# Performance work log

Hardware: AMD Instinct MI355X
Metric: run time of the kernel (lower is better)

## Reference

```python
import jax, jax.numpy as jnp
import numpy as np

BODY = 10      # inds_objs[0][0]
FEAT = 15      # len(inds_objs[0])
NOBJ = 8
HALF = 130     # dimo // 2
B = 65536


def _obj_idx():
    # column indices for each object's features: [NOBJ, 2*FEAT]
    base = BODY + FEAT * np.arange(NOBJ)[:, None] + np.arange(FEAT)[None, :]  # [NOBJ, FEAT]
    return jnp.asarray(np.concatenate([base, base + HALF], axis=1))           # [NOBJ, 30]


def setup_inputs() -> dict:
    key = jax.random.key(0)
    ks = jax.random.split(key, 9)
    def w(k, shape):
        fan_in = shape[0]
        return jax.random.normal(k, shape, jnp.float32) * (1.0 / np.sqrt(fan_in))
    return {
        "o": jax.random.normal(ks[0], (B, 260), jnp.float32),
        "g": jax.random.normal(ks[1], (B, 100), jnp.float32),
        "W_cast": w(ks[2], (100, 50)), "b_cast": jnp.zeros((50,), jnp.float32),
        "W_a0": w(ks[3], (50, 256)),   "b_a0": jnp.zeros((256,), jnp.float32),
        "W_a1": w(ks[4], (256, 400)),  "b_a1": jnp.zeros((400,), jnp.float32),
        "W_p0": w(ks[5], (400, 256)),  "b_p0": jnp.zeros((256,), jnp.float32),
        "W_p1": w(ks[6], (256, 256)),  "b_p1": jnp.zeros((256,), jnp.float32),
        "W_p2": w(ks[7], (256, 8)),    "b_p2": jnp.zeros((8,), jnp.float32),
    }


def reference(o, g, W_cast, b_cast, W_a0, b_a0, W_a1, b_a1,
              W_p0, b_p0, W_p1, b_p1, W_p2, b_p2):
    # attention gate from goal encoding: [B, 50]
    attention = jax.nn.sigmoid(g @ W_cast + b_cast)
    # body features (pos + vel halves): [B, 20]
    obs_body = jnp.concatenate([o[:, :BODY], o[:, HALF:HALF + BODY]], axis=1)
    # per-object features gathered in one shot: [B, NOBJ, 30]
    obs_obj = o[:, _obj_idx()]
    # concat body with each object: [B, NOBJ, 50]
    x = jnp.concatenate(
        [jnp.broadcast_to(obs_body[:, None, :], (o.shape[0], NOBJ, 2 * BODY)), obs_obj],
        axis=2)
    # elementwise attention gate (shared across objects)
    x = x * attention[:, None, :]
    # fc_actor: 50 -> 256 (relu) -> 400, then extra relu from forward()
    h = jax.nn.relu(jnp.einsum('bnd,dh->bnh', x, W_a0) + b_a0)
    y = jax.nn.relu(jnp.einsum('bnh,hk->bnk', h, W_a1) + b_a1)
    # deepset sum over objects: [B, 400]
    input_pi = y.sum(axis=1)
    # fc_pi: 400 -> 256 (relu) -> 256 (relu) -> 8, then tanh
    p = jax.nn.relu(input_pi @ W_p0 + b_p0)
    p = jax.nn.relu(p @ W_p1 + b_p1)
    return jnp.tanh(p @ W_p2 + b_p2)
```

## Files before the change

### kernel.cpp

```cpp
#include <hip/hip_runtime.h>
#include <hip/hip_bf16.h>

typedef _Float16 f16;
typedef f16 v8h __attribute__((ext_vector_type(8)));
typedef float v4f __attribute__((ext_vector_type(4)));
typedef unsigned short u16;

__device__ __forceinline__ u16 f2h(float f) {
  f16 h = (f16)f;
  return __builtin_bit_cast(unsigned short, h);
}
__device__ __forceinline__ float h2f(u16 u) {
  f16 h = __builtin_bit_cast(f16, u);
  return (float)h;
}
#define MFMA16(a, b, c) __builtin_amdgcn_mfma_f32_16x16x32_f16((a), (b), (c), 0, 0, 0)

__global__ void prep_weights(const float* __restrict__ Wc, const float* __restrict__ Wa0,
                             const float* __restrict__ Wa1, const float* __restrict__ Wp0,
                             const float* __restrict__ Wp1, const float* __restrict__ Wp2,
                             u16* __restrict__ ws) {
  int idx = blockIdx.x * 256 + threadIdx.x;
  float v;
  if (idx < 8192) {
    int n = idx >> 7, k = idx & 127;
    v = (n < 50 && k < 100) ? Wc[k * 50 + n] : 0.f;
  } else if (idx < 24576) {
    int i = idx - 8192; int n = i >> 6, k = i & 63;
    v = (k < 50) ? Wa0[k * 256 + n] : 0.f;
  } else if (idx < 126976) {
    int i = idx - 24576; int n = i >> 8, k = i & 255;
    v = Wa1[k * 400 + n];
  } else if (idx < 233472) {
    int i = idx - 126976; int n = i / 416, k = i - n * 416;
    v = (k < 400) ? Wp0[k * 256 + n] : 0.f;
  } else if (idx < 299008) {
    int i = idx - 233472; int n = i >> 8, k = i & 255;
    v = Wp1[k * 256 + n];
  } else if (idx < 303104) {
    int i = idx - 299008; int n = i >> 8, k = i & 255;
    v = (n < 8) ? Wp2[k * 8 + n] : 0.f;
  } else {
    return;
  }
  ws[idx] = f2h(v);
}

__global__ __launch_bounds__(1024) void actor_kernel(
    const float* __restrict__ o, const float* __restrict__ g,
    const float* __restrict__ b_cast, const float* __restrict__ b_a0,
    const float* __restrict__ b_a1, const float* __restrict__ b_p0,
    const float* __restrict__ b_p1, const float* __restrict__ b_p2,
    const u16* __restrict__ wsb, float* __restrict__ out) {
  __shared__ __align__(16) char smem[54272];
  u16* sAtt = (u16*)smem;
  u16* sG   = (u16*)(smem + 7168);
  u16* sX   = (u16*)(smem + 7168);
  u16* sH   = (u16*)(smem + 16384);
  u16* sY   = (u16*)smem;
  u16* sP   = (u16*)smem;

  const u16* WcT  = wsb;
  const u16* Wa0T = wsb + 8192;
  const u16* Wa1T = wsb + 24576;
  const u16* Wp0T = wsb + 126976;
  const u16* Wp1T = wsb + 233472;
  const u16* Wp2T = wsb + 299008;

  const int tid  = threadIdx.x;
  const int lane = tid & 63;
  const int w    = tid >> 6;
  const int nl   = lane & 15;
  const int q    = lane >> 4;
  const int row0 = blockIdx.x * 64;

  for (int idx = tid; idx < 64 * 128; idx += 1024) {
    int r = idx >> 7, c = idx & 127;
    float v = (c < 100) ? __builtin_nontemporal_load(&g[(row0 + r) * 100 + c]) : 0.f;
    sG[r * 136 + c] = f2h(v);
  }
  __syncthreads();

  {
    const int rb = w >> 2, nb = w & 3;
    const int col = nb * 16 + nl;
    v4f acc = {};
#pragma unroll
    for (int kb = 0; kb < 4; ++kb) {
      v8h bh = *(const v8h*)(WcT + col * 128 + kb * 32 + q * 8);
      v8h a  = *(const v8h*)&sG[(rb * 16 + nl) * 136 + kb * 32 + q * 8];
      acc = MFMA16(a, bh, acc);
    }
    if (col < 50) {
      float bias = b_cast[col];
#pragma unroll
      for (int rg = 0; rg < 4; ++rg) {
        float v = acc[rg] + bias;
        v = 1.f / (1.f + __expf(-v));
        sAtt[(rb * 16 + q * 4 + rg) * 56 + col] = f2h(v);
      }
    }
  }
  __syncthreads();

  for (int idx = tid; idx < 64 * 20; idx += 1024) {
    int r = idx / 20, c = idx - r * 20;
    int src = (c < 10) ? c : (c + 120);
    float v = __builtin_nontemporal_load(&o[(row0 + r) * 260 + src]) * h2f(sAtt[r * 56 + c]);
    sX[r * 72 + c] = f2h(v);
  }
  for (int idx = tid; idx < 64 * 14; idx += 1024) {
    int r = idx / 14, c = idx - r * 14;
    sX[r * 72 + 50 + c] = 0;
  }

  const int  nb0  = w;
  const int  nb1  = w + 16;
  const bool has1 = (nb1 < 25);
  const float biasA0  = b_a0[w * 16 + nl];
  const float biasA10 = b_a1[nb0 * 16 + nl];
  const float biasA11 = has1 ? b_a1[nb1 * 16 + nl] : 0.f;
  v4f y0[4] = {};
  v4f y1[4] = {};

  for (int obj = 0; obj < 8; ++obj) {
    for (int idx = tid; idx < 64 * 30; idx += 1024) {
      int r = idx / 30, j = idx - r * 30;
      int src = (j < 15) ? (10 + 15 * obj + j) : (125 + 15 * obj + j);
      float v = __builtin_nontemporal_load(&o[(row0 + r) * 260 + src]) * h2f(sAtt[r * 56 + 20 + j]);
      sX[r * 72 + 20 + j] = f2h(v);
    }
    __syncthreads();

    {
      v4f acc[4] = {};
#pragma unroll
      for (int kb = 0; kb < 2; ++kb) {
        v8h b0 = *(const v8h*)(Wa0T + (w * 16 + nl) * 64 + kb * 32 + q * 8);
#pragma unroll
        for (int rb = 0; rb < 4; ++rb) {
          v8h a = *(const v8h*)&sX[(rb * 16 + nl) * 72 + kb * 32 + q * 8];
          acc[rb] = MFMA16(a, b0, acc[rb]);
        }
      }
      const int col = w * 16 + nl;
#pragma unroll
      for (int rb = 0; rb < 4; ++rb)
#pragma unroll
        for (int rg = 0; rg < 4; ++rg) {
          float v = acc[rb][rg] + biasA0;
          v = v > 0.f ? v : 0.f;
          sH[(rb * 16 + q * 4 + rg) * 264 + col] = f2h(v);
        }
    }
    __syncthreads();

    {
      v4f t0[4] = {}, t1[4] = {};
#pragma unroll
      for (int kb = 0; kb < 8; ++kb) {
        v8h b0 = *(const v8h*)(Wa1T + (nb0 * 16 + nl) * 256 + kb * 32 + q * 8);
        v8h b1;
        if (has1) b1 = *(const v8h*)(Wa1T + (nb1 * 16 + nl) * 256 + kb * 32 + q * 8);
#pragma unroll
        for (int rb = 0; rb < 4; ++rb) {
          v8h a = *(const v8h*)&sH[(rb * 16 + nl) * 264 + kb * 32 + q * 8];
          t0[rb] = MFMA16(a, b0, t0[rb]);
          if (has1) t1[rb] = MFMA16(a, b1, t1[rb]);
        }
      }
#pragma unroll
      for (int rb = 0; rb < 4; ++rb)
#pragma unroll
        for (int rg = 0; rg < 4; ++rg) {
          float v = t0[rb][rg] + biasA10;
          y0[rb][rg] += (v > 0.f ? v : 0.f);
        }
      if (has1) {
#pragma unroll
        for (int rb = 0; rb < 4; ++rb)
#pragma unroll
          for (int rg = 0; rg < 4; ++rg) {
            float v = t1[rb][rg] + biasA11;
            y1[rb][rg] += (v > 0.f ? v : 0.f);
          }
      }
    }
  }
  __syncthreads();

  for (int idx = tid; idx < 64 * 16; idx += 1024) {
    int r = idx >> 4, c = idx & 15;
    sY[r * 424 + 400 + c] = 0;
  }
#pragma unroll
  for (int rb = 0; rb < 4; ++rb)
#pragma unroll
    for (int rg = 0; rg < 4; ++rg) {
      const int row = rb * 16 + q * 4 + rg;
      sY[row * 424 + nb0 * 16 + nl] = f2h(y0[rb][rg]);
      if (has1) sY[row * 424 + nb1 * 16 + nl] = f2h(y1[rb][rg]);
    }
  __syncthreads();

  v4f p0acc[4] = {};
#pragma unroll
  for (int kb = 0; kb < 13; ++kb) {
    v8h b0 = *(const v8h*)(Wp0T + (w * 16 + nl) * 416 + kb * 32 + q * 8);
#pragma unroll
    for (int rb = 0; rb < 4; ++rb) {
      v8h a = *(const v8h*)&sY[(rb * 16 + nl) * 424 + kb * 32 + q * 8];
      p0acc[rb] = MFMA16(a, b0, p0acc[rb]);
    }
  }
  __syncthreads();
  {
    const int col = w * 16 + nl;
    float bias = b_p0[col];
#pragma unroll
    for (int rb = 0; rb < 4; ++rb)
#pragma unroll
      for (int rg = 0; rg < 4; ++rg) {
        float v = p0acc[rb][rg] + bias;
        v = v > 0.f ? v : 0.f;
        sP[(rb * 16 + q * 4 + rg) * 264 + col] = f2h(v);
      }
  }
  __syncthreads();

  v4f p1acc[4] = {};
#pragma unroll
  for (int kb = 0; kb < 8; ++kb) {
    v8h b0 = *(const v8h*)(Wp1T + (w * 16 + nl) * 256 + kb * 32 + q * 8);
#pragma unroll
    for (int rb = 0; rb < 4; ++rb) {
      v8h a = *(const v8h*)&sP[(rb * 16 + nl) * 264 + kb * 32 + q * 8];
      p1acc[rb] = MFMA16(a, b0, p1acc[rb]);
    }
  }
  __syncthreads();
  {
    const int col = w * 16 + nl;
    float bias = b_p1[col];
#pragma unroll
    for (int rb = 0; rb < 4; ++rb)
#pragma unroll
      for (int rg = 0; rg < 4; ++rg) {
        float v = p1acc[rb][rg] + bias;
        v = v > 0.f ? v : 0.f;
        sP[(rb * 16 + q * 4 + rg) * 264 + col] = f2h(v);
      }
  }
  __syncthreads();

  if (w < 4) {
    v4f acc = {};
#pragma unroll
    for (int kb = 0; kb < 8; ++kb) {
      v8h a = *(const v8h*)&sP[(w * 16 + nl) * 264 + kb * 32 + q * 8];
      v8h b = *(const v8h*)(Wp2T + nl * 256 + kb * 32 + q * 8);
      acc = MFMA16(a, b, acc);
    }
    if (nl < 8) {
      float bias = b_p2[nl];
#pragma unroll
      for (int rg = 0; rg < 4; ++rg)
        __builtin_nontemporal_store(tanhf(acc[rg] + bias),
                                    &out[(row0 + w * 16 + q * 4 + rg) * 8 + nl]);
    }
  }
}

extern "C" void kernel_launch(void* const* d_in, const int* in_sizes, int n_in,
                              void* d_out, int out_size, void* d_ws, size_t ws_size,
                              hipStream_t stream) {
  const float* o   = (const float*)d_in[0];
  const float* g   = (const float*)d_in[1];
  const float* Wc  = (const float*)d_in[2];
  const float* bc  = (const float*)d_in[3];
  const float* Wa0 = (const float*)d_in[4];
  const float* ba0 = (const float*)d_in[5];
  const float* Wa1 = (const float*)d_in[6];
  const float* ba1 = (const float*)d_in[7];
  const float* Wp0 = (const float*)d_in[8];
  const float* bp0 = (const float*)d_in[9];
  const float* Wp1 = (const float*)d_in[10];
  const float* bp1 = (const float*)d_in[11];
  const float* Wp2 = (const float*)d_in[12];
  const float* bp2 = (const float*)d_in[13];
  u16* ws = (u16*)d_ws;
  float* out = (float*)d_out;

  int rows = in_sizes[0] / 260;

  prep_weights<<<1184, 256, 0, stream>>>(Wc, Wa0, Wa1, Wp0, Wp1, Wp2, ws);
  actor_kernel<<<rows / 64, 1024, 0, stream>>>(o, g, bc, ba0, ba1, bp0, bp1, bp2, ws, out);
}
```

Baseline: 379.3 us.

## Preload all object features into LDS, double-buffer hidden, transpose MFMA outputs for packed stores

```diff
diff --git a/kernel.cpp b/kernel.cpp
--- a/kernel.cpp
+++ b/kernel.cpp
@@ -4,7 +4,10 @@
 typedef _Float16 f16;
 typedef f16 v8h __attribute__((ext_vector_type(8)));
 typedef float v4f __attribute__((ext_vector_type(4)));
+typedef float v2f __attribute__((ext_vector_type(2)));
+typedef unsigned int v2u __attribute__((ext_vector_type(2)));
 typedef unsigned short u16;
+typedef unsigned int u32;
 
 __device__ __forceinline__ u16 f2h(float f) {
   f16 h = (f16)f;
@@ -13,6 +16,9 @@
 __device__ __forceinline__ float h2f(u16 u) {
   f16 h = __builtin_bit_cast(f16, u);
   return (float)h;
+}
+__device__ __forceinline__ u32 pk2(float a, float b) {
+  return (u32)f2h(a) | ((u32)f2h(b) << 16);
 }
 #define MFMA16(a, b, c) __builtin_amdgcn_mfma_f32_16x16x32_f16((a), (b), (c), 0, 0, 0)
 
@@ -52,13 +58,14 @@
     const float* __restrict__ b_a1, const float* __restrict__ b_p0,
     const float* __restrict__ b_p1, const float* __restrict__ b_p2,
     const u16* __restrict__ wsb, float* __restrict__ out) {
-  __shared__ __align__(16) char smem[54272];
+  __shared__ __align__(16) char smem[148480];
   u16* sAtt = (u16*)smem;
   u16* sG   = (u16*)(smem + 7168);
-  u16* sX   = (u16*)(smem + 7168);
-  u16* sH   = (u16*)(smem + 16384);
-  u16* sY   = (u16*)smem;
-  u16* sP   = (u16*)smem;
+  u16* sX0  = (u16*)(smem + 7168);
+  u16* sH0  = (u16*)(smem + 80896);
+  u16* sH1  = (u16*)(smem + 114688);
+  u16* sY   = (u16*)(smem + 7168);
+  u16* sP   = (u16*)(smem + 7168);
 
   const u16* WcT  = wsb;
   const u16* Wa0T = wsb + 8192;
@@ -74,63 +81,96 @@
   const int q    = lane >> 4;
   const int row0 = blockIdx.x * 64;
 
+  v2f fo1[4], fo2[4];
+  v2f fb = {};
+#pragma unroll
+  for (int i = 0; i < 4; ++i) {
+    int idx = tid + i * 1024;
+    if (idx < 3840) {
+      int r = idx / 60, c2 = idx - r * 60;
+      const float* rp = o + (size_t)(row0 + r) * 260;
+      fo1[i] = *(const v2f*)(rp + 10 + 2 * c2);
+      fo2[i] = *(const v2f*)(rp + 140 + 2 * c2);
+    }
+  }
+  if (tid < 640) {
+    int r = tid / 10, hh = tid - r * 10;
+    const float* rp = o + (size_t)(row0 + r) * 260;
+    int src = (hh < 5) ? (2 * hh) : (2 * hh + 120);
+    fb = *(const v2f*)(rp + src);
+  }
+
   for (int idx = tid; idx < 64 * 128; idx += 1024) {
     int r = idx >> 7, c = idx & 127;
-    float v = (c < 100) ? __builtin_nontemporal_load(&g[(row0 + r) * 100 + c]) : 0.f;
+    float v = (c < 100) ? __builtin_nontemporal_load(&g[(size_t)(row0 + r) * 100 + c]) : 0.f;
     sG[r * 136 + c] = f2h(v);
   }
   __syncthreads();
 
   {
-    const int rb = w >> 2, nb = w & 3;
-    const int col = nb * 16 + nl;
+    const int rb = w >> 2, nbq = w & 3;
     v4f acc = {};
 #pragma unroll
     for (int kb = 0; kb < 4; ++kb) {
-      v8h bh = *(const v8h*)(WcT + col * 128 + kb * 32 + q * 8);
+      v8h bh = *(const v8h*)(WcT + (nbq * 16 + nl) * 128 + kb * 32 + q * 8);
       v8h a  = *(const v8h*)&sG[(rb * 16 + nl) * 136 + kb * 32 + q * 8];
-      acc = MFMA16(a, bh, acc);
-    }
-    if (col < 50) {
-      float bias = b_cast[col];
-#pragma unroll
-      for (int rg = 0; rg < 4; ++rg) {
-        float v = acc[rg] + bias;
+      acc = MFMA16(bh, a, acc);
+    }
+    const int row = rb * 16 + nl;
+#pragma unroll
+    for (int rg = 0; rg < 4; ++rg) {
+      int col = nbq * 16 + q * 4 + rg;
+      if (col < 50) {
+        float v = acc[rg] + b_cast[col];
         v = 1.f / (1.f + __expf(-v));
-        sAtt[(rb * 16 + q * 4 + rg) * 56 + col] = f2h(v);
-      }
-    }
-  }
-  __syncthreads();
-
-  for (int idx = tid; idx < 64 * 20; idx += 1024) {
-    int r = idx / 20, c = idx - r * 20;
-    int src = (c < 10) ? c : (c + 120);
-    float v = __builtin_nontemporal_load(&o[(row0 + r) * 260 + src]) * h2f(sAtt[r * 56 + c]);
-    sX[r * 72 + c] = f2h(v);
-  }
-  for (int idx = tid; idx < 64 * 14; idx += 1024) {
-    int r = idx / 14, c = idx - r * 14;
-    sX[r * 72 + 50 + c] = 0;
-  }
+        sAtt[row * 56 + col] = f2h(v);
+      }
+    }
+  }
+  __syncthreads();
+
+#pragma unroll
+  for (int i = 0; i < 4; ++i) {
+    int idx = tid + i * 1024;
+    if (idx < 3840) {
+      int r = idx / 60, c2 = idx - r * 60;
+      int cc0 = 2 * c2, cc1 = cc0 + 1;
+      int ob0 = cc0 / 15, j0 = cc0 - ob0 * 15;
+      int ob1 = cc1 / 15, j1 = cc1 - ob1 * 15;
+      u16* xr = sX0 + r * 72;
+      xr[ob0 * 4608 + 20 + j0] = f2h(fo1[i][0] * h2f(sAtt[r * 56 + 20 + j0]));
+      xr[ob1 * 4608 + 20 + j1] = f2h(fo1[i][1] * h2f(sAtt[r * 56 + 20 + j1]));
+      xr[ob0 * 4608 + 35 + j0] = f2h(fo2[i][0] * h2f(sAtt[r * 56 + 35 + j0]));
+      xr[ob1 * 4608 + 35 + j1] = f2h(fo2[i][1] * h2f(sAtt[r * 56 + 35 + j1]));
+    }
+  }
+  if (tid < 640) {
+    int r = tid / 10, hh = tid - r * 10;
+    int c0 = 2 * hh, c1 = c0 + 1;
+    u16 x0 = f2h(fb[0] * h2f(sAtt[r * 56 + c0]));
+    u16 x1 = f2h(fb[1] * h2f(sAtt[r * 56 + c1]));
+    u16* xr = sX0 + r * 72;
+#pragma unroll
+    for (int ob = 0; ob < 8; ++ob) {
+      xr[ob * 4608 + c0] = x0;
+      xr[ob * 4608 + c1] = x1;
+    }
+  }
+  for (int idx = tid; idx < 64 * 8 * 7; idx += 1024) {
+    int t = idx; int uu = t % 7; t /= 7; int ob = t & 7; int r = t >> 3;
+    *(u32*)&sX0[ob * 4608 + r * 72 + 50 + 2 * uu] = 0;
+  }
+  __syncthreads();
 
   const int  nb0  = w;
   const int  nb1  = w + 16;
   const bool has1 = (nb1 < 25);
-  const float biasA0  = b_a0[w * 16 + nl];
-  const float biasA10 = b_a1[nb0 * 16 + nl];
-  const float biasA11 = has1 ? b_a1[nb1 * 16 + nl] : 0.f;
   v4f y0[4] = {};
   v4f y1[4] = {};
 
   for (int obj = 0; obj < 8; ++obj) {
-    for (int idx = tid; idx < 64 * 30; idx += 1024) {
-      int r = idx / 30, j = idx - r * 30;
-      int src = (j < 15) ? (10 + 15 * obj + j) : (125 + 15 * obj + j);
-      float v = __builtin_nontemporal_load(&o[(row0 + r) * 260 + src]) * h2f(sAtt[r * 56 + 20 + j]);
-      sX[r * 72 + 20 + j] = f2h(v);
-    }
-    __syncthreads();
+    u16* sHd = (obj & 1) ? sH1 : sH0;
+    const u16* sXo = sX0 + obj * 4608;
 
     {
       v4f acc[4] = {};
@@ -139,19 +179,20 @@
         v8h b0 = *(const v8h*)(Wa0T + (w * 16 + nl) * 64 + kb * 32 + q * 8);
 #pragma unroll
         for (int rb = 0; rb < 4; ++rb) {
-          v8h a = *(const v8h*)&sX[(rb * 16 + nl) * 72 + kb * 32 + q * 8];
-          acc[rb] = MFMA16(a, b0, acc[rb]);
+          v8h a = *(const v8h*)&sXo[(rb * 16 + nl) * 72 + kb * 32 + q * 8];
+          acc[rb] = MFMA16(b0, a, acc[rb]);
         }
       }
-      const int col = w * 16 + nl;
-#pragma unroll
-      for (int rb = 0; rb < 4; ++rb)
-#pragma unroll
-        for (int rg = 0; rg < 4; ++rg) {
-          float v = acc[rb][rg] + biasA0;
-          v = v > 0.f ? v : 0.f;
-          sH[(rb * 16 + q * 4 + rg) * 264 + col] = f2h(v);
-        }
+      v4f bs = *(const v4f*)&b_a0[w * 16 + q * 4];
+#pragma unroll
+      for (int rb = 0; rb < 4; ++rb) {
+        float v0 = acc[rb][0] + bs[0]; v0 = v0 > 0.f ? v0 : 0.f;
+        float v1 = acc[rb][1] + bs[1]; v1 = v1 > 0.f ? v1 : 0.f;
+        float v2 = acc[rb][2] + bs[2]; v2 = v2 > 0.f ? v2 : 0.f;
+        float v3 = acc[rb][3] + bs[3]; v3 = v3 > 0.f ? v3 : 0.f;
+        v2u pk; pk[0] = pk2(v0, v1); pk[1] = pk2(v2, v3);
+        *(v2u*)&sHd[(rb * 16 + nl) * 264 + w * 16 + q * 4] = pk;
+      }
     }
     __syncthreads();
 
@@ -164,24 +205,26 @@
         if (has1) b1 = *(const v8h*)(Wa1T + (nb1 * 16 + nl) * 256 + kb * 32 + q * 8);
 #pragma unroll
         for (int rb = 0; rb < 4; ++rb) {
-          v8h a = *(const v8h*)&sH[(rb * 16 + nl) * 264 + kb * 32 + q * 8];
-          t0[rb] = MFMA16(a, b0, t0[rb]);
-          if (has1) t1[rb] = MFMA16(a, b1, t1[rb]);
+          v8h a = *(const v8h*)&sHd[(rb * 16 + nl) * 264 + kb * 32 + q * 8];
+          t0[rb] = MFMA16(b0, a, t0[rb]);
+          if (has1) t1[rb] = MFMA16(b1, a, t1[rb]);
         }
       }
+      v4f bs0 = *(const v4f*)&b_a1[nb0 * 16 + q * 4];
 #pragma unroll
       for (int rb = 0; rb < 4; ++rb)
 #pragma unroll
         for (int rg = 0; rg < 4; ++rg) {
-          float v = t0[rb][rg] + biasA10;
+          float v = t0[rb][rg] + bs0[rg];
           y0[rb][rg] += (v > 0.f ? v : 0.f);
         }
       if (has1) {
+        v4f bs1 = *(const v4f*)&b_a1[nb1 * 16 + q * 4];
 #pragma unroll
         for (int rb = 0; rb < 4; ++rb)
 #pragma unroll
           for (int rg = 0; rg < 4; ++rg) {
-            float v = t1[rb][rg] + biasA11;
+            float v = t1[rb][rg] + bs1[rg];
             y1[rb][rg] += (v > 0.f ? v : 0.f);
           }
       }
@@ -189,18 +232,20 @@
   }
   __syncthreads();
 
-  for (int idx = tid; idx < 64 * 16; idx += 1024) {
-    int r = idx >> 4, c = idx & 15;
-    sY[r * 424 + 400 + c] = 0;
-  }
-#pragma unroll
-  for (int rb = 0; rb < 4; ++rb)
-#pragma unroll
-    for (int rg = 0; rg < 4; ++rg) {
-      const int row = rb * 16 + q * 4 + rg;
-      sY[row * 424 + nb0 * 16 + nl] = f2h(y0[rb][rg]);
-      if (has1) sY[row * 424 + nb1 * 16 + nl] = f2h(y1[rb][rg]);
-    }
+  if (tid < 512) {
+    int r = tid >> 3, uu = tid & 7;
+    *(u32*)&sY[r * 424 + 400 + 2 * uu] = 0;
+  }
+#pragma unroll
+  for (int rb = 0; rb < 4; ++rb) {
+    const int row = rb * 16 + nl;
+    v2u pk0; pk0[0] = pk2(y0[rb][0], y0[rb][1]); pk0[1] = pk2(y0[rb][2], y0[rb][3]);
+    *(v2u*)&sY[row * 424 + nb0 * 16 + q * 4] = pk0;
+    if (has1) {
+      v2u pk1; pk1[0] = pk2(y1[rb][0], y1[rb][1]); pk1[1] = pk2(y1[rb][2], y1[rb][3]);
+      *(v2u*)&sY[row * 424 + nb1 * 16 + q * 4] = pk1;
+    }
+  }
   __syncthreads();
 
   v4f p0acc[4] = {};
@@ -210,21 +255,21 @@
 #pragma unroll
     for (int rb = 0; rb < 4; ++rb) {
       v8h a = *(const v8h*)&sY[(rb * 16 + nl) * 424 + kb * 32 + q * 8];
-      p0acc[rb] = MFMA16(a, b0, p0acc[rb]);
+      p0acc[rb] = MFMA16(b0, a, p0acc[rb]);
     }
   }
   __syncthreads();
   {
-    const int col = w * 16 + nl;
-    float bias = b_p0[col];
-#pragma unroll
-    for (int rb = 0; rb < 4; ++rb)
-#pragma unroll
-      for (int rg = 0; rg < 4; ++rg) {
-        float v = p0acc[rb][rg] + bias;
-        v = v > 0.f ? v : 0.f;
-        sP[(rb * 16 + q * 4 + rg) * 264 + col] = f2h(v);
-      }
+    v4f bs = *(const v4f*)&b_p0[w * 16 + q * 4];
+#pragma unroll
+    for (int rb = 0; rb < 4; ++rb) {
+      float v0 = p0acc[rb][0] + bs[0]; v0 = v0 > 0.f ? v0 : 0.f;
+      float v1 = p0acc[rb][1] + bs[1]; v1 = v1 > 0.f ? v1 : 0.f;
+      float v2 = p0acc[rb][2] + bs[2]; v2 = v2 > 0.f ? v2 : 0.f;
+      float v3 = p0acc[rb][3] + bs[3]; v3 = v3 > 0.f ? v3 : 0.f;
+      v2u pk; pk[0] = pk2(v0, v1); pk[1] = pk2(v2, v3);
+      *(v2u*)&sP[(rb * 16 + nl) * 264 + w * 16 + q * 4] = pk;
+    }
   }
   __syncthreads();
 
@@ -235,21 +280,21 @@
 #pragma unroll
     for (int rb = 0; rb < 4; ++rb) {
       v8h a = *(const v8h*)&sP[(rb * 16 + nl) * 264 + kb * 32 + q * 8];
-      p1acc[rb] = MFMA16(a, b0, p1acc[rb]);
+      p1acc[rb] = MFMA16(b0, a, p1acc[rb]);
     }
   }
   __syncthreads();
   {
-    const int col = w * 16 + nl;
-    float bias = b_p1[col];
-#pragma unroll
-    for (int rb = 0; rb < 4; ++rb)
-#pragma unroll
-      for (int rg = 0; rg < 4; ++rg) {
-        float v = p1acc[rb][rg] + bias;
-        v = v > 0.f ? v : 0.f;
-        sP[(rb * 16 + q * 4 + rg) * 264 + col] = f2h(v);
-      }
+    v4f bs = *(const v4f*)&b_p1[w * 16 + q * 4];
+#pragma unroll
+    for (int rb = 0; rb < 4; ++rb) {
+      float v0 = p1acc[rb][0] + bs[0]; v0 = v0 > 0.f ? v0 : 0.f;
+      float v1 = p1acc[rb][1] + bs[1]; v1 = v1 > 0.f ? v1 : 0.f;
+      float v2 = p1acc[rb][2] + bs[2]; v2 = v2 > 0.f ? v2 : 0.f;
+      float v3 = p1acc[rb][3] + bs[3]; v3 = v3 > 0.f ? v3 : 0.f;
+      v2u pk; pk[0] = pk2(v0, v1); pk[1] = pk2(v2, v3);
+      *(v2u*)&sP[(rb * 16 + nl) * 264 + w * 16 + q * 4] = pk;
+    }
   }
   __syncthreads();
 
@@ -259,14 +304,14 @@
     for (int kb = 0; kb < 8; ++kb) {
       v8h a = *(const v8h*)&sP[(w * 16 + nl) * 264 + kb * 32 + q * 8];
       v8h b = *(const v8h*)(Wp2T + nl * 256 + kb * 32 + q * 8);
-      acc = MFMA16(a, b, acc);
-    }
-    if (nl < 8) {
-      float bias = b_p2[nl];
-#pragma unroll
-      for (int rg = 0; rg < 4; ++rg)
-        __builtin_nontemporal_store(tanhf(acc[rg] + bias),
-                                    &out[(row0 + w * 16 + q * 4 + rg) * 8 + nl]);
+      acc = MFMA16(b, a, acc);
+    }
+    if (q < 2) {
+      v4f bp = *(const v4f*)&b_p2[q * 4];
+      v4f r;
+#pragma unroll
+      for (int rg = 0; rg < 4; ++rg) r[rg] = tanhf(acc[rg] + bp[rg]);
+      *(v4f*)&out[(size_t)(row0 + w * 16 + nl) * 8 + q * 4] = r;
     }
   }
 }
```

Result: slower. 980.8 us (+158.5%).

## Preload all object features into LDS and double-buffer hidden activations

Applied to the files above, without the earlier changes.

```diff
diff --git a/kernel.cpp b/kernel.cpp
--- a/kernel.cpp
+++ b/kernel.cpp
@@ -4,7 +4,9 @@
 typedef _Float16 f16;
 typedef f16 v8h __attribute__((ext_vector_type(8)));
 typedef float v4f __attribute__((ext_vector_type(4)));
+typedef float v2f __attribute__((ext_vector_type(2)));
 typedef unsigned short u16;
+typedef unsigned int u32;
 
 __device__ __forceinline__ u16 f2h(float f) {
   f16 h = (f16)f;
@@ -52,13 +54,14 @@
     const float* __restrict__ b_a1, const float* __restrict__ b_p0,
     const float* __restrict__ b_p1, const float* __restrict__ b_p2,
     const u16* __restrict__ wsb, float* __restrict__ out) {
-  __shared__ __align__(16) char smem[54272];
+  __shared__ __align__(16) char smem[148480];
   u16* sAtt = (u16*)smem;
   u16* sG   = (u16*)(smem + 7168);
-  u16* sX   = (u16*)(smem + 7168);
-  u16* sH   = (u16*)(smem + 16384);
-  u16* sY   = (u16*)smem;
-  u16* sP   = (u16*)smem;
+  u16* sX0  = (u16*)(smem + 7168);
+  u16* sH0  = (u16*)(smem + 80896);
+  u16* sH1  = (u16*)(smem + 114688);
+  u16* sY   = (u16*)(smem + 7168);
+  u16* sP   = (u16*)(smem + 7168);
 
   const u16* WcT  = wsb;
   const u16* Wa0T = wsb + 8192;
@@ -76,14 +79,14 @@
 
   for (int idx = tid; idx < 64 * 128; idx += 1024) {
     int r = idx >> 7, c = idx & 127;
-    float v = (c < 100) ? __builtin_nontemporal_load(&g[(row0 + r) * 100 + c]) : 0.f;
+    float v = (c < 100) ? __builtin_nontemporal_load(&g[(size_t)(row0 + r) * 100 + c]) : 0.f;
     sG[r * 136 + c] = f2h(v);
   }
   __syncthreads();
 
   {
-    const int rb = w >> 2, nb = w & 3;
-    const int col = nb * 16 + nl;
+    const int rb = w >> 2, nbq = w & 3;
+    const int col = nbq * 16 + nl;
     v4f acc = {};
 #pragma unroll
     for (int kb = 0; kb < 4; ++kb) {
@@ -103,34 +106,54 @@
   }
   __syncthreads();
 
-  for (int idx = tid; idx < 64 * 20; idx += 1024) {
-    int r = idx / 20, c = idx - r * 20;
-    int src = (c < 10) ? c : (c + 120);
-    float v = __builtin_nontemporal_load(&o[(row0 + r) * 260 + src]) * h2f(sAtt[r * 56 + c]);
-    sX[r * 72 + c] = f2h(v);
-  }
-  for (int idx = tid; idx < 64 * 14; idx += 1024) {
-    int r = idx / 14, c = idx - r * 14;
-    sX[r * 72 + 50 + c] = 0;
-  }
+#pragma unroll
+  for (int i = 0; i < 4; ++i) {
+    int idx = tid + i * 1024;
+    if (idx < 3840) {
+      int r = idx / 60, c2 = idx - r * 60;
+      const float* rp = o + (size_t)(row0 + r) * 260;
+      v2f f1 = *(const v2f*)(rp + 10 + 2 * c2);
+      v2f f2 = *(const v2f*)(rp + 140 + 2 * c2);
+      int cc0 = 2 * c2, cc1 = cc0 + 1;
+      int ob0 = cc0 / 15, j0 = cc0 - ob0 * 15;
+      int ob1 = cc1 / 15, j1 = cc1 - ob1 * 15;
+      u16* xr = sX0 + r * 72;
+      xr[ob0 * 4608 + 20 + j0] = f2h(f1[0] * h2f(sAtt[r * 56 + 20 + j0]));
+      xr[ob1 * 4608 + 20 + j1] = f2h(f1[1] * h2f(sAtt[r * 56 + 20 + j1]));
+      xr[ob0 * 4608 + 35 + j0] = f2h(f2[0] * h2f(sAtt[r * 56 + 35 + j0]));
+      xr[ob1 * 4608 + 35 + j1] = f2h(f2[1] * h2f(sAtt[r * 56 + 35 + j1]));
+    }
+  }
+  if (tid < 640) {
+    int r = tid / 10, hh = tid - r * 10;
+    const float* rp = o + (size_t)(row0 + r) * 260;
+    int src = (hh < 5) ? (2 * hh) : (2 * hh + 120);
+    v2f fb = *(const v2f*)(rp + src);
+    int c0 = 2 * hh, c1 = c0 + 1;
+    u16 x0 = f2h(fb[0] * h2f(sAtt[r * 56 + c0]));
+    u16 x1 = f2h(fb[1] * h2f(sAtt[r * 56 + c1]));
+    u16* xr = sX0 + r * 72;
+#pragma unroll
+    for (int ob = 0; ob < 8; ++ob) {
+      xr[ob * 4608 + c0] = x0;
+      xr[ob * 4608 + c1] = x1;
+    }
+  }
+  for (int idx = tid; idx < 64 * 8 * 7; idx += 1024) {
+    int t = idx; int uu = t % 7; t /= 7; int ob = t & 7; int r = t >> 3;
+    *(u32*)&sX0[ob * 4608 + r * 72 + 50 + 2 * uu] = 0;
+  }
+  __syncthreads();
 
   const int  nb0  = w;
   const int  nb1  = w + 16;
   const bool has1 = (nb1 < 25);
-  const float biasA0  = b_a0[w * 16 + nl];
-  const float biasA10 = b_a1[nb0 * 16 + nl];
-  const float biasA11 = has1 ? b_a1[nb1 * 16 + nl] : 0.f;
   v4f y0[4] = {};
   v4f y1[4] = {};
 
   for (int obj = 0; obj < 8; ++obj) {
-    for (int idx = tid; idx < 64 * 30; idx += 1024) {
-      int r = idx / 30, j = idx - r * 30;
-      int src = (j < 15) ? (10 + 15 * obj + j) : (125 + 15 * obj + j);
-      float v = __builtin_nontemporal_load(&o[(row0 + r) * 260 + src]) * h2f(sAtt[r * 56 + 20 + j]);
-      sX[r * 72 + 20 + j] = f2h(v);
-    }
-    __syncthreads();
+    u16* sHd = (obj & 1) ? sH1 : sH0;
+    const u16* sXo = sX0 + obj * 4608;
 
     {
       v4f acc[4] = {};
@@ -139,18 +162,19 @@
         v8h b0 = *(const v8h*)(Wa0T + (w * 16 + nl) * 64 + kb * 32 + q * 8);
 #pragma unroll
         for (int rb = 0; rb < 4; ++rb) {
-          v8h a = *(const v8h*)&sX[(rb * 16 + nl) * 72 + kb * 32 + q * 8];
+          v8h a = *(const v8h*)&sXo[(rb * 16 + nl) * 72 + kb * 32 + q * 8];
           acc[rb] = MFMA16(a, b0, acc[rb]);
         }
       }
       const int col = w * 16 + nl;
+      float bias = b_a0[col];
 #pragma unroll
       for (int rb = 0; rb < 4; ++rb)
 #pragma unroll
         for (int rg = 0; rg < 4; ++rg) {
-          float v = acc[rb][rg] + biasA0;
+          float v = acc[rb][rg] + bias;
           v = v > 0.f ? v : 0.f;
-          sH[(rb * 16 + q * 4 + rg) * 264 + col] = f2h(v);
+          sHd[(rb * 16 + q * 4 + rg) * 264 + col] = f2h(v);
         }
     }
     __syncthreads();
@@ -164,24 +188,26 @@
         if (has1) b1 = *(const v8h*)(Wa1T + (nb1 * 16 + nl) * 256 + kb * 32 + q * 8);
 #pragma unroll
         for (int rb = 0; rb < 4; ++rb) {
-          v8h a = *(const v8h*)&sH[(rb * 16 + nl) * 264 + kb * 32 + q * 8];
+          v8h a = *(const v8h*)&sHd[(rb * 16 + nl) * 264 + kb * 32 + q * 8];
           t0[rb] = MFMA16(a, b0, t0[rb]);
           if (has1) t1[rb] = MFMA16(a, b1, t1[rb]);
         }
       }
+      float bias0 = b_a1[nb0 * 16 + nl];
 #pragma unroll
       for (int rb = 0; rb < 4; ++rb)
 #pragma unroll
         for (int rg = 0; rg < 4; ++rg) {
-          float v = t0[rb][rg] + biasA10;
+          float v = t0[rb][rg] + bias0;
           y0[rb][rg] += (v > 0.f ? v : 0.f);
         }
       if (has1) {
+        float bias1 = b_a1[nb1 * 16 + nl];
 #pragma unroll
         for (int rb = 0; rb < 4; ++rb)
 #pragma unroll
           for (int rg = 0; rg < 4; ++rg) {
-            float v = t1[rb][rg] + biasA11;
+            float v = t1[rb][rg] + bias1;
             y1[rb][rg] += (v > 0.f ? v : 0.f);
           }
       }
@@ -266,7 +292,7 @@
 #pragma unroll
       for (int rg = 0; rg < 4; ++rg)
         __builtin_nontemporal_store(tanhf(acc[rg] + bias),
-                                    &out[(row0 + w * 16 + q * 4 + rg) * 8 + nl]);
+                                    &out[(size_t)(row0 + w * 16 + q * 4 + rg) * 8 + nl]);
     }
   }
 }
```

Measured after the change: 341.9 us (median of 3 runs). 1.11x faster.
